# Kernel tuning notes

Hardware: AMD Instinct MI355X
Metric: run time of the kernel (lower is better)

Reference implementation:

```python
import jax, jax.numpy as jnp
import numpy as np

BINS = 32  # position_bins


def setup_inputs() -> dict:
    key = jax.random.key(0)
    ks = jax.random.split(key, 7)
    N, IN, E = 1024, 21, 128
    return {
        "target_feat": jax.random.normal(ks[0], (N, IN), dtype=jnp.float32),
        "residue_index": jnp.arange(N, dtype=jnp.int64),
        "Wa": jax.random.normal(ks[1], (E, IN), dtype=jnp.float32) * 0.1,
        "ba": jax.random.normal(ks[2], (E,), dtype=jnp.float32) * 0.1,
        "Wb": jax.random.normal(ks[3], (E, IN), dtype=jnp.float32) * 0.1,
        "bb": jax.random.normal(ks[4], (E,), dtype=jnp.float32) * 0.1,
        "Wp": jax.random.normal(ks[5], (E, 2 * BINS + 1), dtype=jnp.float32) * 0.1,
        "bp": jax.random.normal(ks[6], (E,), dtype=jnp.float32) * 0.1,
    }


def reference(target_feat, residue_index, Wa, ba, Wb, bb, Wp, bp):
    # Linear projections: [N, E]
    a = target_feat @ Wa.T + ba
    b = target_feat @ Wb.T + bb
    # Relative position bucket: [N, N] int in [0, 2*BINS]
    d = residue_index[:, None] - residue_index[None, :]
    d = jnp.clip(d, -BINS, BINS) + BINS
    # one_hot(d) @ Wp.T + bp  ==  row gather from Wp.T (fused, no one-hot)
    p = jnp.take(Wp.T, d, axis=0) + bp  # [N, N, E]
    # Outer broadcast sum z = a_i + b_j plus position term
    return a[:, None, :] + b[None, :, :] + p
```

## Files before the change

### kernel.cpp

```cpp
#include <hip/hip_runtime.h>

#define NN    1024
#define INF   21
#define EE    128
#define NB    65
#define BINSV 32

typedef float f32x4 __attribute__((ext_vector_type(4)));

__global__ __launch_bounds__(128) void prep_kernel(
    const float* __restrict__ tf,
    const float* __restrict__ Wa, const float* __restrict__ ba,
    const float* __restrict__ Wb, const float* __restrict__ bb,
    const float* __restrict__ Wp, const float* __restrict__ bp,
    float* __restrict__ a, float* __restrict__ b, float* __restrict__ ptab) {
  const int e = threadIdx.x;
  if (blockIdx.x < NN) {
    const int i = blockIdx.x;
    __shared__ float row[INF];
    if (e < INF) row[e] = tf[i * INF + e];
    __syncthreads();
    float sa = ba[e];
    float sb = bb[e];
#pragma unroll
    for (int k = 0; k < INF; ++k) {
      float r = row[k];
      sa = fmaf(r, Wa[e * INF + k], sa);
      sb = fmaf(r, Wb[e * INF + k], sb);
    }
    a[i * EE + e] = sa;
    b[i * EE + e] = sb;
  } else {
    const int d = blockIdx.x - NN;
    ptab[d * EE + e] = Wp[e * NB + d] + bp[e];
  }
}

__global__ __launch_bounds__(512) void fill_kernel(
    const float* __restrict__ a, const float* __restrict__ b,
    const float* __restrict__ ptab, const int* __restrict__ ri,
    float* __restrict__ out) {
  __shared__ int sri[NN];
  const int tid = threadIdx.x;
  for (int t = tid; t < NN; t += 512) sri[t] = ri[t];
  __syncthreads();

  const int i  = blockIdx.x;
  const int e4 = tid & 31;
  const int jg = tid >> 5;

  const f32x4* __restrict__ b4 = reinterpret_cast<const f32x4*>(b);
  const f32x4* __restrict__ p4 = reinterpret_cast<const f32x4*>(ptab);

  const f32x4 av = reinterpret_cast<const f32x4*>(a + i * EE)[e4];
  const int rii = sri[i];
  f32x4* outrow = reinterpret_cast<f32x4*>(out + (size_t)i * NN * EE);

  auto bin = [&](int j) {
    int d = rii - sri[j];
    d = (d < -BINSV) ? -BINSV : (d > BINSV ? BINSV : d);
    return d + BINSV;
  };

  int j = (i + jg) & (NN - 1);
  f32x4 bv = b4[j * 32 + e4];

  for (int t = 1; t < NN / 16; ++t) {
    const int jn = (i + jg + 16 * t) & (NN - 1);
    f32x4 bvn = b4[jn * 32 + e4];
    const f32x4 o = av + bv + p4[bin(j) * 32 + e4];
    __builtin_nontemporal_store(o, outrow + j * 32 + e4);
    j = jn; bv = bvn;
  }
  const f32x4 o = av + bv + p4[bin(j) * 32 + e4];
  __builtin_nontemporal_store(o, outrow + j * 32 + e4);
}

extern "C" void kernel_launch(void* const* d_in, const int* in_sizes, int n_in,
                              void* d_out, int out_size, void* d_ws, size_t ws_size,
                              hipStream_t stream) {
  const float* tf = (const float*)d_in[0];
  const int*   ri = (const int*)d_in[1];
  const float* Wa = (const float*)d_in[2];
  const float* ba = (const float*)d_in[3];
  const float* Wb = (const float*)d_in[4];
  const float* bb = (const float*)d_in[5];
  const float* Wp = (const float*)d_in[6];
  const float* bp = (const float*)d_in[7];
  float* out = (float*)d_out;

  float* ws   = (float*)d_ws;
  float* a    = ws;
  float* b    = ws + NN * EE;
  float* ptab = ws + 2 * NN * EE;

  prep_kernel<<<NN + NB, 128, 0, stream>>>(tf, Wa, ba, Wb, bb, Wp, bp, a, b, ptab);
  fill_kernel<<<NN, 512, 0, stream>>>(a, b, ptab, ri, out);
}
```

Baseline: 114.5 us.

## Remap fill kernel so each wave writes contiguous 1KB chunks across strided rows

Reorganizes the work split in the fill kernel: each wave now owns a fixed pair of columns j and a residue class of rows i, loading b once and iterating over 64 rows with stride 16. With this mapping, consecutive waves in a block write adjacent 1KB output segments, so each block's stores sweep a contiguous address region per iteration instead of each block filling one full output row. The intent is to improve DRAM write locality and concurrency across channels. It trades this for per-iteration loads of a and an LDS lookup of the residue index for i.

Measured after the change: 110.8 us. 1.03x faster.

```diff
diff --git a/kernel.cpp b/kernel.cpp
--- a/kernel.cpp
+++ b/kernel.cpp
@@ -45,35 +45,33 @@
   for (int t = tid; t < NN; t += 512) sri[t] = ri[t];
   __syncthreads();
 
-  const int i  = blockIdx.x;
-  const int e4 = tid & 31;
-  const int jg = tid >> 5;
+  const int lane = tid & 63;
+  const int hi   = lane >> 5;
+  const int e4   = lane & 31;
+  const int w    = blockIdx.x * 8 + (tid >> 6);
+  const int jp   = w & 511;
+  const int ic   = w >> 9;
+  const int j    = 2 * jp + hi;
 
-  const f32x4* __restrict__ b4 = reinterpret_cast<const f32x4*>(b);
+  const f32x4* __restrict__ a4 = reinterpret_cast<const f32x4*>(a);
   const f32x4* __restrict__ p4 = reinterpret_cast<const f32x4*>(ptab);
 
-  const f32x4 av = reinterpret_cast<const f32x4*>(a + i * EE)[e4];
-  const int rii = sri[i];
-  f32x4* outrow = reinterpret_cast<f32x4*>(out + (size_t)i * NN * EE);
+  const f32x4 bv = reinterpret_cast<const f32x4*>(b + j * EE)[e4];
+  const int rj = sri[j];
 
-  auto bin = [&](int j) {
-    int d = rii - sri[j];
-    d = (d < -BINSV) ? -BINSV : (d > BINSV ? BINSV : d);
-    return d + BINSV;
-  };
+  f32x4* __restrict__ o4 = reinterpret_cast<f32x4*>(out);
 
-  int j = (i + jg) & (NN - 1);
-  f32x4 bv = b4[j * 32 + e4];
-
-  for (int t = 1; t < NN / 16; ++t) {
-    const int jn = (i + jg + 16 * t) & (NN - 1);
-    f32x4 bvn = b4[jn * 32 + e4];
-    const f32x4 o = av + bv + p4[bin(j) * 32 + e4];
-    __builtin_nontemporal_store(o, outrow + j * 32 + e4);
-    j = jn; bv = bvn;
+#pragma unroll 4
+  for (int t = 0; t < 64; ++t) {
+    const int i = t * 16 + ic;
+    const f32x4 av = a4[i * 32 + e4];
+    int d = sri[i] - rj;
+    d = min(max(d, -BINSV), BINSV) + BINSV;
+    const f32x4 pv = p4[d * 32 + e4];
+    const f32x4 o = av + bv + pv;
+    const size_t u = (size_t)t * 8192 + w;
+    __builtin_nontemporal_store(o, o4 + u * 64 + hi * 32 + e4);
   }
-  const f32x4 o = av + bv + p4[bin(j) * 32 + e4];
-  __builtin_nontemporal_store(o, outrow + j * 32 + e4);
 }
 
 extern "C" void kernel_launch(void* const* d_in, const int* in_sizes, int n_in,
```

## Remap fill waves to contiguous half-rows with double-buffered b/ptab prefetch

Applied to the files above, without the earlier changes.

Each wavefront now owns a contiguous half-row of the output (512 j values) instead of blocks striding j in a rotated order. Loads of b and the position table are software-pipelined two steps ahead. The grid drops to 256 blocks of 512 threads. The goal is more sequential store streams and hidden gather latency for this bandwidth-bound fill, at the cost of some wasted wrapped prefetch loads at the tail.

Result: slower. 126.1 us (+10.1%).

```diff
diff --git a/kernel.cpp b/kernel.cpp
--- a/kernel.cpp
+++ b/kernel.cpp
@@ -45,35 +45,48 @@
   for (int t = tid; t < NN; t += 512) sri[t] = ri[t];
   __syncthreads();
 
-  const int i  = blockIdx.x;
-  const int e4 = tid & 31;
-  const int jg = tid >> 5;
+  const int lane = tid & 63;
+  const int hi   = lane >> 5;
+  const int e4   = lane & 31;
+  const int w    = blockIdx.x * 8 + (tid >> 6);
+  const int i    = w >> 1;
+  const int j0   = (w & 1) << 9;
 
   const f32x4* __restrict__ b4 = reinterpret_cast<const f32x4*>(b);
   const f32x4* __restrict__ p4 = reinterpret_cast<const f32x4*>(ptab);
 
   const f32x4 av = reinterpret_cast<const f32x4*>(a + i * EE)[e4];
   const int rii = sri[i];
-  f32x4* outrow = reinterpret_cast<f32x4*>(out + (size_t)i * NN * EE);
 
-  auto bin = [&](int j) {
+  f32x4* __restrict__ o4 =
+      reinterpret_cast<f32x4*>(out) + (size_t)w * 512 * 32 + hi * 32 + e4;
+
+  auto dbin = [&](int j) {
     int d = rii - sri[j];
-    d = (d < -BINSV) ? -BINSV : (d > BINSV ? BINSV : d);
-    return d + BINSV;
+    return min(max(d, -BINSV), BINSV) + BINSV;
   };
 
-  int j = (i + jg) & (NN - 1);
-  f32x4 bv = b4[j * 32 + e4];
+  {
+    const int jA = j0 + hi;
+    f32x4 bv0 = b4[jA * 32 + e4];
+    f32x4 pv0 = p4[dbin(jA) * 32 + e4];
+    const int jB = j0 + 2 + hi;
+    f32x4 bv1 = b4[jB * 32 + e4];
+    f32x4 pv1 = p4[dbin(jB) * 32 + e4];
 
-  for (int t = 1; t < NN / 16; ++t) {
-    const int jn = (i + jg + 16 * t) & (NN - 1);
-    f32x4 bvn = b4[jn * 32 + e4];
-    const f32x4 o = av + bv + p4[bin(j) * 32 + e4];
-    __builtin_nontemporal_store(o, outrow + j * 32 + e4);
-    j = jn; bv = bvn;
+    for (int t = 0; t < 256; t += 2) {
+      const int jn0 = (j0 + 2 * (t + 2) + hi) & (NN - 1);
+      const f32x4 nb0 = b4[jn0 * 32 + e4];
+      const f32x4 np0 = p4[dbin(jn0) * 32 + e4];
+      __builtin_nontemporal_store(av + bv0 + pv0, o4 + (size_t)t * 64);
+      const int jn1 = (j0 + 2 * (t + 3) + hi) & (NN - 1);
+      const f32x4 nb1 = b4[jn1 * 32 + e4];
+      const f32x4 np1 = p4[dbin(jn1) * 32 + e4];
+      __builtin_nontemporal_store(av + bv1 + pv1, o4 + (size_t)(t + 1) * 64);
+      bv0 = nb0; pv0 = np0;
+      bv1 = nb1; pv1 = np1;
+    }
   }
-  const f32x4 o = av + bv + p4[bin(j) * 32 + e4];
-  __builtin_nontemporal_store(o, outrow + j * 32 + e4);
 }
 
 extern "C" void kernel_launch(void* const* d_in, const int* in_sizes, int n_in,
@@ -95,5 +108,5 @@
   float* ptab = ws + 2 * NN * EE;
 
   prep_kernel<<<NN + NB, 128, 0, stream>>>(tf, Wa, ba, Wb, bb, Wp, bp, a, b, ptab);
-  fill_kernel<<<NN, 512, 0, stream>>>(a, b, ptab, ri, out);
+  fill_kernel<<<256, 512, 0, stream>>>(a, b, ptab, ri, out);
 }
```
